# Kernel optimization log

Measured on AMD Instinct MI355X. Metric: run time of the kernel, lower is better.

Reference implementation:

```python
import jax, jax.numpy as jnp
import numpy as np

N_NODES = 8192
N_EDGES = 524288
N_PAIRS = 262144
N_TYPES = 86


def _gcn_conv(x, W, b, src, dst, n):
    # PyG GCNConv: transform, add self-loops, symmetric degree normalization,
    # scatter-add aggregation at destination nodes.
    xw = x @ W  # [N, F_out]
    loop = jnp.arange(n, dtype=src.dtype)
    s = jnp.concatenate([src, loop])
    d = jnp.concatenate([dst, loop])
    deg = jax.ops.segment_sum(jnp.ones(d.shape, xw.dtype), d, num_segments=n)
    dinv = jnp.where(deg > 0, jax.lax.rsqrt(deg), 0.0)  # deg^{-1/2}, 0 for isolated
    coef = dinv[s] * dinv[d]  # [E+N]
    out = jax.ops.segment_sum(xw[s] * coef[:, None], d, num_segments=n)
    return out + b


def setup_inputs() -> dict:
    key = jax.random.key(0)
    ks = jax.random.split(key, 10)
    x = jax.random.normal(ks[0], (N_NODES, N_NODES), dtype=jnp.float32)
    edge_index = jax.random.randint(ks[1], (2, N_EDGES), 0, N_NODES, dtype=jnp.int32)
    drug1_idx = jax.random.randint(ks[2], (N_PAIRS,), 0, N_NODES, dtype=jnp.int32)
    drug2_idx = jax.random.randint(ks[3], (N_PAIRS,), 0, N_NODES, dtype=jnp.int32)
    W1 = jax.random.normal(ks[4], (N_NODES, 128), dtype=jnp.float32) / np.sqrt(N_NODES)
    b1 = jnp.zeros((128,), jnp.float32)
    W2 = jax.random.normal(ks[5], (128, 64), dtype=jnp.float32) / np.sqrt(128.0)
    b2 = jnp.zeros((64,), jnp.float32)
    Wfc = jax.random.normal(ks[6], (128, N_TYPES), dtype=jnp.float32) / np.sqrt(128.0)
    bfc = jnp.zeros((N_TYPES,), jnp.float32)
    return {"x": x, "edge_index": edge_index, "drug1_idx": drug1_idx,
            "drug2_idx": drug2_idx, "W1": W1, "b1": b1, "W2": W2, "b2": b2,
            "Wfc": Wfc, "bfc": bfc}


def reference(x, edge_index, drug1_idx, drug2_idx, W1, b1, W2, b2, Wfc, bfc):
    n = x.shape[0]
    src, dst = edge_index[0], edge_index[1]
    h = jax.nn.relu(_gcn_conv(x, W1, b1, src, dst, n))
    # dropout p=0.3 is identity at inference (training=False)
    h = jax.nn.relu(_gcn_conv(h, W2, b2, src, dst, n))
    combined = jnp.concatenate([h[drug1_idx], h[drug2_idx]], axis=1)  # [P, 128]
    return jax.nn.sigmoid(combined @ Wfc + bfc)
```

## Files before the change

kernel.cpp:

```cpp
#include <hip/hip_runtime.h>
#include <math.h>
#include <stdint.h>
#include <stddef.h>

#define N_NODES 8192
#define N_EDGES 524288
#define N_PAIRS 262144
#define N_TYPES 86
#define F1 128
#define F2 64

typedef unsigned short ushort_t;
typedef unsigned int uint_t;
typedef __attribute__((ext_vector_type(8))) short bfrag;
typedef __attribute__((ext_vector_type(4))) uint_t ufrag;
typedef __attribute__((ext_vector_type(4))) float ffrag;

typedef __attribute__((address_space(3))) char lds_char;
typedef __attribute__((address_space(1))) const char g_char;

__device__ __forceinline__ void gload16(const void* g, void* l) {
  __builtin_amdgcn_global_load_lds((const g_char*)g, (lds_char*)l, 16, 0, 0);
}

__device__ inline ushort_t f2bf(float f) {
  uint_t u = __float_as_uint(f);
  uint_t r = u + 0x7fffu + ((u >> 16) & 1u);
  return (ushort_t)(r >> 16);
}
__device__ inline float bf2f(ushort_t h) {
  return __uint_as_float(((uint_t)h) << 16);
}

__device__ __forceinline__ bfrag cvtfrag(float4 a, float4 b) {
  uint_t h0, h1, h2, h3;
  asm("v_cvt_pk_bf16_f32 %0, %1, %2" : "=v"(h0) : "v"(a.x), "v"(a.y));
  asm("v_cvt_pk_bf16_f32 %0, %1, %2" : "=v"(h1) : "v"(a.z), "v"(a.w));
  asm("v_cvt_pk_bf16_f32 %0, %1, %2" : "=v"(h2) : "v"(b.x), "v"(b.y));
  asm("v_cvt_pk_bf16_f32 %0, %1, %2" : "=v"(h3) : "v"(b.z), "v"(b.w));
  ufrag u;
  u.x = h0; u.y = h1; u.z = h2; u.w = h3;
  return __builtin_bit_cast(bfrag, u);
}


__global__ void zero_k(int* __restrict__ p) {
  p[blockIdx.x * 256 + threadIdx.x] = 0;
}

__global__ void count_deg_k(const int* __restrict__ dst, int* __restrict__ cnt) {
  int e = blockIdx.x * blockDim.x + threadIdx.x;
  if (e < N_EDGES) atomicAdd(&cnt[dst[e]], 1);
}

__global__ void scan_k(const int* __restrict__ cnt, int* __restrict__ rp,
                       int* __restrict__ fill, float* __restrict__ dinv) {
  __shared__ int s[1024];
  int t = threadIdx.x;
  int v[8];
  int sum = 0;
#pragma unroll
  for (int i = 0; i < 8; i++) {
    v[i] = cnt[t * 8 + i];
    dinv[t * 8 + i] = 1.0f / sqrtf((float)(v[i] + 1));
    sum += v[i];
  }
  s[t] = sum;
  __syncthreads();
  for (int off = 1; off < 1024; off <<= 1) {
    int add = (t >= off) ? s[t - off] : 0;
    __syncthreads();
    s[t] += add;
    __syncthreads();
  }
  int excl = s[t] - sum;
#pragma unroll
  for (int i = 0; i < 8; i++) {
    rp[t * 8 + i] = excl;
    fill[t * 8 + i] = excl;
    excl += v[i];
  }
  if (t == 1023) rp[N_NODES] = excl;
}

__global__ void scatter_k(const int* __restrict__ src, const int* __restrict__ dst,
                          int* fill, int* __restrict__ csr) {
  int e = blockIdx.x * blockDim.x + threadIdx.x;
  if (e < N_EDGES) {
    int d = dst[e];
    int pos = atomicAdd(&fill[d], 1);
    csr[pos] = src[e];
  }
}


__global__ __launch_bounds__(256) void w1t_k(const float* __restrict__ W1,
                                             ushort_t* __restrict__ W1t) {
  __shared__ ushort_t lh[32 * 65];
  int tid = threadIdx.x;
  int k0 = blockIdx.x * 64;
  int n0 = blockIdx.y * 32;
#pragma unroll
  for (int i = 0; i < 8; i++) {
    int c = tid + 256 * i;
    int kr = c >> 5, nc = c & 31;
    lh[nc * 65 + kr] = f2bf(W1[(size_t)(k0 + kr) * F1 + n0 + nc]);
  }
  __syncthreads();
  {
    int c = tid;
    int nr = c >> 3, kc = c & 7;
    uint4 u;
    u.x = (uint_t)lh[nr * 65 + kc * 8 + 0] | ((uint_t)lh[nr * 65 + kc * 8 + 1] << 16);
    u.y = (uint_t)lh[nr * 65 + kc * 8 + 2] | ((uint_t)lh[nr * 65 + kc * 8 + 3] << 16);
    u.z = (uint_t)lh[nr * 65 + kc * 8 + 4] | ((uint_t)lh[nr * 65 + kc * 8 + 5] << 16);
    u.w = (uint_t)lh[nr * 65 + kc * 8 + 6] | ((uint_t)lh[nr * 65 + kc * 8 + 7] << 16);
    *(uint4*)(W1t + (size_t)(n0 + nr) * N_NODES + k0 + kc * 8) = u;
  }
}


#define BLDS(b) ((b) * 8192)

#define SCHED0 __builtin_amdgcn_sched_barrier(0)
#define WAITVM(N)  do { asm volatile("s_waitcnt vmcnt(" #N ")" ::: "memory"); SCHED0; } while (0)

__global__ __launch_bounds__(256, 2) void gemm1_mfma_k(const float* __restrict__ x,
                                                       const ushort_t* __restrict__ W1t,
                                                       float* __restrict__ part, int kspan) {
  __shared__ __align__(16) char lds[16384];
  int tid = threadIdx.x;
  int wave = tid >> 6, lane = tid & 63;
  int wr = wave >> 1, wc = wave & 1;
  int lrow = lane & 15, kgrp = lane >> 4;
  int m_blk = blockIdx.y * 128;
  int kbase = blockIdx.x * kspan;
  int ktiles = kspan >> 5;
  int s0 = (5 * blockIdx.y + 3 * blockIdx.x) & (ktiles - 1);

  const float* ap0 = x + (size_t)(m_blk + wr * 64 + 0 * 16 + lrow) * N_NODES + kgrp * 8;
  const float* ap1 = x + (size_t)(m_blk + wr * 64 + 1 * 16 + lrow) * N_NODES + kgrp * 8;
  const float* ap2 = x + (size_t)(m_blk + wr * 64 + 2 * 16 + lrow) * N_NODES + kgrp * 8;
  const float* ap3 = x + (size_t)(m_blk + wr * 64 + 3 * 16 + lrow) * N_NODES + kgrp * 8;

  int bq = wave;
  int b_row = bq * 32 + (lane >> 2);
  int b_kel = ((lane & 3) ^ ((lane >> 2) & 3)) << 3;

  ffrag acc[4][4];
#pragma unroll
  for (int mi = 0; mi < 4; mi++)
#pragma unroll
    for (int ni = 0; ni < 4; ni++) acc[mi][ni] = (ffrag)(0.0f);

  float4 sP[8], sQ[8];
  bfrag afr[4];

#define ISSUE_A(KO, SET)                                                             \
  {                                                                                  \
    SET[0] = *(const float4*)(ap0 + (KO));                                           \
    SET[1] = *(const float4*)(ap0 + (KO) + 4);                                       \
    SET[2] = *(const float4*)(ap1 + (KO));                                           \
    SET[3] = *(const float4*)(ap1 + (KO) + 4);                                       \
    SET[4] = *(const float4*)(ap2 + (KO));                                           \
    SET[5] = *(const float4*)(ap2 + (KO) + 4);                                       \
    SET[6] = *(const float4*)(ap3 + (KO));                                           \
    SET[7] = *(const float4*)(ap3 + (KO) + 4);                                       \
  }

#define CONV(SET)                                                                    \
  {                                                                                  \
    afr[0] = cvtfrag(SET[0], SET[1]);                                                \
    afr[1] = cvtfrag(SET[2], SET[3]);                                                \
    afr[2] = cvtfrag(SET[4], SET[5]);                                                \
    afr[3] = cvtfrag(SET[6], SET[7]);                                                \
  }

#define ISSUE_B(K0, BSEL)                                                            \
  {                                                                                  \
    _Pragma("unroll") for (int i = 0; i < 2; i++) {                                  \
      const ushort_t* gp = W1t + (size_t)(b_row + i * 16) * N_NODES + (K0) + b_kel;  \
      gload16(gp, lds + BLDS(BSEL) + bq * 2048 + i * 1024);                          \
    }                                                                                \
  }

#define COMPUTE(BSEL)                                                                \
  {                                                                                  \
    bfrag bh[4];                                                                     \
    _Pragma("unroll") for (int ni = 0; ni < 4; ni++) {                               \
      int brow = wc * 64 + ni * 16 + lrow;                                           \
      uint_t boff = brow * 64 + ((kgrp ^ (brow & 3)) << 4);                          \
      bh[ni] = *(const bfrag*)(lds + BLDS(BSEL) + boff);                             \
    }                                                                                \
    _Pragma("unroll") for (int mi = 0; mi < 4; mi++) {                               \
      _Pragma("unroll") for (int ni = 0; ni < 4; ni++) {                             \
        acc[mi][ni] = __builtin_amdgcn_mfma_f32_16x16x32_bf16(afr[mi], bh[ni], acc[mi][ni], 0, 0, 0); \
      }                                                                              \
    }                                                                                \
  }

#define NXT(p) ((p) + 1 == ktiles ? 0 : (p) + 1)

  int p1 = s0;
  int p2 = NXT(p1);
  ISSUE_A(kbase + (p1 << 5), sP);
  SCHED0;
  ISSUE_B(kbase + (p1 << 5), 0);
  SCHED0;
  ISSUE_A(kbase + (p2 << 5), sQ);
  WAITVM(10);
  CONV(sP);
  WAITVM(8);
  __builtin_amdgcn_s_barrier();
  SCHED0;

  for (int it = 0; it < ktiles; it += 2) {
    {
      int pB = NXT(p1), pA = NXT(pB);
      ISSUE_B(kbase + (pB << 5), 1);
      SCHED0;
      ISSUE_A(kbase + (pA << 5), sP);
      SCHED0;
      __builtin_amdgcn_s_setprio(1);
      COMPUTE(0);
      __builtin_amdgcn_s_setprio(0);
      WAITVM(10);
      CONV(sQ);
      WAITVM(8);
      __builtin_amdgcn_s_barrier();
      SCHED0;
      p1 = pB;
    }
    {
      int pB = NXT(p1), pA = NXT(pB);
      ISSUE_B(kbase + (pB << 5), 0);
      SCHED0;
      ISSUE_A(kbase + (pA << 5), sQ);
      SCHED0;
      __builtin_amdgcn_s_setprio(1);
      COMPUTE(1);
      __builtin_amdgcn_s_setprio(0);
      WAITVM(10);
      CONV(sP);
      WAITVM(8);
      __builtin_amdgcn_s_barrier();
      SCHED0;
      p1 = pB;
    }
  }

  float* outp = part + (size_t)blockIdx.x * (N_NODES * F1);
#pragma unroll
  for (int mi = 0; mi < 4; mi++) {
#pragma unroll
    for (int ni = 0; ni < 4; ni++) {
      int col = wc * 64 + ni * 16 + lrow;
#pragma unroll
      for (int r = 0; r < 4; r++) {
        int row = m_blk + wr * 64 + mi * 16 + kgrp * 4 + r;
        outp[(size_t)row * F1 + col] = acc[mi][ni][r];
      }
    }
  }
#undef ISSUE_A
#undef CONV
#undef ISSUE_B
#undef COMPUTE
#undef NXT
}

__global__ void reduceS_k(const float* __restrict__ part, float* __restrict__ xw1, int S) {
  int i = blockIdx.x * blockDim.x + threadIdx.x;
  float4 a = ((const float4*)part)[i];
  for (int s = 1; s < S; s++) {
    float4 b = ((const float4*)(part + (size_t)s * N_NODES * F1))[i];
    a.x += b.x; a.y += b.y; a.z += b.z; a.w += b.w;
  }
  ((float4*)xw1)[i] = a;
}


template <int F>
__global__ void agg_k(const float* __restrict__ xw, const int* __restrict__ csr,
                      const int* __restrict__ rp, const float* __restrict__ dinv,
                      const float* __restrict__ bias, float* __restrict__ hout) {
  int node = blockIdx.x;
  int f = threadIdx.x;
  __shared__ int sidx[F];
  __shared__ float sdv[F];
  int beg = rp[node], end = rp[node + 1];
  float acc = 0.f;
  for (int base = beg; base < end; base += F) {
    int n = end - base;
    if (n > F) n = F;
    __syncthreads();
    if (f < n) {
      int s = csr[base + f];
      sidx[f] = s;
      sdv[f] = dinv[s];
    }
    __syncthreads();
    for (int i = 0; i < n; i++) acc += xw[(size_t)sidx[i] * F + f] * sdv[i];
  }
  float dv = dinv[node];
  float v = (acc + xw[(size_t)node * F + f] * dv) * dv + bias[f];
  hout[(size_t)node * F + f] = v > 0.f ? v : 0.f;
}


__global__ __launch_bounds__(256) void gemm2_k(const float* __restrict__ h1,
                                               const float* __restrict__ W2,
                                               float* __restrict__ xw2) {
  __shared__ float W2s[F1 * F2];
  __shared__ float As[16 * F1];
  int tid = threadIdx.x;
  int r0 = blockIdx.x * 16;
#pragma unroll
  for (int j = 0; j < 8; j++)
    ((float4*)W2s)[tid + 256 * j] = ((const float4*)W2)[tid + 256 * j];
#pragma unroll
  for (int j = 0; j < 2; j++)
    ((float4*)As)[tid + 256 * j] = ((const float4*)(h1 + (size_t)r0 * F1))[tid + 256 * j];
  __syncthreads();
  int r = tid >> 4, c4 = tid & 15;
  float4 acc = make_float4(0.f, 0.f, 0.f, 0.f);
#pragma unroll 8
  for (int k = 0; k < F1; k++) {
    float a = As[r * F1 + k];
    float4 bv = *(float4*)&W2s[k * F2 + 4 * c4];
    acc.x += a * bv.x; acc.y += a * bv.y; acc.z += a * bv.z; acc.w += a * bv.w;
  }
  *(float4*)&xw2[(size_t)(r0 + r) * F2 + 4 * c4] = acc;
}


__global__ void pboth_k(const float* __restrict__ h2, const float* __restrict__ Wfc,
                        float* __restrict__ P) {
  __shared__ float hs[64 * 16];
  int tid = threadIdx.x;
  int r0 = blockIdx.x * 16;
  for (int idx = tid; idx < 256; idx += 192) {
    int row = idx >> 4, k4 = idx & 15;
    float4 h = *(const float4*)&h2[(size_t)(r0 + row) * F2 + 4 * k4];
    hs[(4 * k4 + 0) * 16 + row] = h.x;
    hs[(4 * k4 + 1) * 16 + row] = h.y;
    hs[(4 * k4 + 2) * 16 + row] = h.z;
    hs[(4 * k4 + 3) * 16 + row] = h.w;
  }
  __syncthreads();
  if (tid < 172) {
    int half = tid < 86 ? 0 : 1;
    int j = tid - 86 * half;
    const float* wp = Wfc + (size_t)(64 * half) * N_TYPES + j;
    float acc[16];
#pragma unroll
    for (int r = 0; r < 16; r++) acc[r] = 0.f;
    for (int k = 0; k < 64; k++) {
      float w = wp[(size_t)k * N_TYPES];
      const float* hk = &hs[k * 16];
#pragma unroll
      for (int r = 0; r < 16; r++) acc[r] += hk[r] * w;
    }
#pragma unroll
    for (int r = 0; r < 16; r++) P[(size_t)(r0 + r) * 172 + tid] = acc[r];
  }
}


__global__ void final_k(const float* __restrict__ P, const int* __restrict__ d1,
                        const int* __restrict__ d2, const float* __restrict__ bfc,
                        float* __restrict__ out) {
  int gid = blockIdx.x * blockDim.x + threadIdx.x;
  if (gid >= N_PAIRS * 43) return;
  int p = gid / 43;
  int j = gid - p * 43;
  int a = d1[p], b = d2[p];
  float2 v1 = *(const float2*)&P[(size_t)a * 172 + 2 * j];
  float2 v2 = *(const float2*)&P[(size_t)b * 172 + 86 + 2 * j];
  float2 bb = *(const float2*)&bfc[2 * j];
  float z0 = v1.x + v2.x + bb.x;
  float z1 = v1.y + v2.y + bb.y;
  float2 o;
  o.x = 1.0f / (1.0f + expf(-z0));
  o.y = 1.0f / (1.0f + expf(-z1));
  *(float2*)&out[(size_t)p * 86 + 2 * j] = o;
}


extern "C" void kernel_launch(void* const* d_in, const int* in_sizes, int n_in,
                              void* d_out, int out_size, void* d_ws, size_t ws_size,
                              hipStream_t stream) {
  const float* x   = (const float*)d_in[0];
  const int*   ei  = (const int*)d_in[1];
  const int*   d1  = (const int*)d_in[2];
  const int*   d2  = (const int*)d_in[3];
  const float* W1  = (const float*)d_in[4];
  const float* b1  = (const float*)d_in[5];
  const float* W2  = (const float*)d_in[6];
  const float* b2  = (const float*)d_in[7];
  const float* Wfc = (const float*)d_in[8];
  const float* bfc = (const float*)d_in[9];
  float* out = (float*)d_out;

  const int* esrc = ei;
  const int* edst = ei + N_EDGES;

  char* w = (char*)d_ws;
  size_t off = 0;
  auto alloc = [&](size_t bytes) -> char* {
    char* p = w + off;
    off += (bytes + 255) & ~(size_t)255;
    return p;
  };
  int*      cnt  = (int*)alloc((size_t)N_NODES * 4);
  float*    dinv = (float*)alloc((size_t)N_NODES * 4);
  int*      rp   = (int*)alloc((size_t)(N_NODES + 1) * 4);
  int*      fill = (int*)alloc((size_t)N_NODES * 4);
  int*      csr  = (int*)alloc((size_t)N_EDGES * 4);
  ushort_t* W1t  = (ushort_t*)alloc((size_t)N_NODES * F1 * 2);
  float*    h1   = (float*)alloc((size_t)N_NODES * F1 * 4);
  float*    xw2  = (float*)alloc((size_t)N_NODES * F2 * 4);
  float*    h2   = (float*)alloc((size_t)N_NODES * F2 * 4);
  float*    P    = (float*)alloc((size_t)N_NODES * 172 * 4);

  size_t partBytes = (size_t)N_NODES * F1 * 4;
  int S = 8;
  while (S > 1 && off + (size_t)S * partBytes > ws_size) S >>= 1;
  float* part = (float*)alloc((size_t)S * partBytes);
  float* xw1 = part;
  if (off > ws_size) return;

  zero_k<<<N_NODES / 256, 256, 0, stream>>>(cnt);
  count_deg_k<<<N_EDGES / 256, 256, 0, stream>>>(edst, cnt);
  scan_k<<<1, 1024, 0, stream>>>(cnt, rp, fill, dinv);
  scatter_k<<<N_EDGES / 256, 256, 0, stream>>>(esrc, edst, fill, csr);

  w1t_k<<<dim3(N_NODES / 64, F1 / 32), 256, 0, stream>>>(W1, W1t);
  gemm1_mfma_k<<<dim3(S, N_NODES / 128), 256, 0, stream>>>(x, W1t, part, N_NODES / S);
  if (S > 1)
    reduceS_k<<<(N_NODES * F1 / 4) / 256, 256, 0, stream>>>(part, xw1, S);
  agg_k<F1><<<N_NODES, F1, 0, stream>>>(xw1, csr, rp, dinv, b1, h1);

  gemm2_k<<<N_NODES / 16, 256, 0, stream>>>(h1, W2, xw2);
  agg_k<F2><<<N_NODES, F2, 0, stream>>>(xw2, csr, rp, dinv, b2, h2);

  pboth_k<<<N_NODES / 16, 192, 0, stream>>>(h2, Wfc, P);
  final_k<<<(N_PAIRS * 43 + 255) / 256, 256, 0, stream>>>(P, d1, d2, bfc, out);
}
```

Measured before the change: 265.5 us.

## Pre-pack x into bf16 tiles in a separate kernel before GEMM1

Adds a pack kernel that reads the fp32 x matrix once, converts it to bf16 and writes it into a tiled layout matching the MFMA fragment order. The GEMM1 kernel then loads ready-made bf16 fragments instead of converting fp32 in the inner loop, and the pipeline drops to simple single-tile prefetch with full vmcnt(0) waits. This costs an extra 256MB read plus 128MB write and a 128MB workspace, and removes the overlap of the previous deeper prefetch, which is a significant risk for a bandwidth-bound GEMM. The split count S is fixed at 8 and no longer adapts to workspace size.

Result: slower. 322.0 us (+21.3%).

```diff
diff --git a/kernel.cpp b/kernel.cpp
--- a/kernel.cpp
+++ b/kernel.cpp
@@ -28,11 +28,8 @@
   uint_t r = u + 0x7fffu + ((u >> 16) & 1u);
   return (ushort_t)(r >> 16);
 }
-__device__ inline float bf2f(ushort_t h) {
-  return __uint_as_float(((uint_t)h) << 16);
-}
-
-__device__ __forceinline__ bfrag cvtfrag(float4 a, float4 b) {
+
+__device__ __forceinline__ ufrag cvt8(float4 a, float4 b) {
   uint_t h0, h1, h2, h3;
   asm("v_cvt_pk_bf16_f32 %0, %1, %2" : "=v"(h0) : "v"(a.x), "v"(a.y));
   asm("v_cvt_pk_bf16_f32 %0, %1, %2" : "=v"(h1) : "v"(a.z), "v"(a.w));
@@ -40,7 +37,7 @@
   asm("v_cvt_pk_bf16_f32 %0, %1, %2" : "=v"(h3) : "v"(b.z), "v"(b.w));
   ufrag u;
   u.x = h0; u.y = h1; u.z = h2; u.w = h3;
-  return __builtin_bit_cast(bfrag, u);
+  return u;
 }
 
 
@@ -120,28 +117,54 @@
 }
 
 
+__global__ __launch_bounds__(256) void pack_k(const float* __restrict__ x,
+                                              ushort_t* __restrict__ xp) {
+  int tid = threadIdx.x;
+  size_t tile = (size_t)(blockIdx.x * 64 + blockIdx.y) * 131072;
+  const float* xb = x + (size_t)(blockIdx.y * 128) * N_NODES + blockIdx.x * 1024;
+  ushort_t* tp = xp + tile;
+#pragma unroll 4
+  for (int i = 0; i < 32; i++) {
+    int c = tid + 256 * i;
+    int row = c >> 6;
+    int kc = c & 63;
+    const float* p = xb + (size_t)row * N_NODES + kc * 16;
+    float4 v0 = *(const float4*)(p + 0);
+    float4 v1 = *(const float4*)(p + 4);
+    float4 v2 = *(const float4*)(p + 8);
+    float4 v3 = *(const float4*)(p + 12);
+    ufrag u0 = cvt8(v0, v1);
+    ufrag u1 = cvt8(v2, v3);
+    int s = kc >> 1;
+    ushort_t* q = tp + s * 4096 + row * 32 + (kc & 1) * 16;
+    *(ufrag*)q = u0;
+    *(ufrag*)(q + 8) = u1;
+  }
+}
+
+
 #define BLDS(b) ((b) * 8192)
-
 #define SCHED0 __builtin_amdgcn_sched_barrier(0)
 #define WAITVM(N)  do { asm volatile("s_waitcnt vmcnt(" #N ")" ::: "memory"); SCHED0; } while (0)
 
-__global__ __launch_bounds__(256, 2) void gemm1_mfma_k(const float* __restrict__ x,
+__global__ __launch_bounds__(256, 2) void gemm1_mfma_k(const ushort_t* __restrict__ xp,
                                                        const ushort_t* __restrict__ W1t,
-                                                       float* __restrict__ part, int kspan) {
+                                                       float* __restrict__ part) {
   __shared__ __align__(16) char lds[16384];
   int tid = threadIdx.x;
   int wave = tid >> 6, lane = tid & 63;
   int wr = wave >> 1, wc = wave & 1;
   int lrow = lane & 15, kgrp = lane >> 4;
   int m_blk = blockIdx.y * 128;
-  int kbase = blockIdx.x * kspan;
-  int ktiles = kspan >> 5;
+  int kbase = blockIdx.x * 1024;
+  const int ktiles = 32;
   int s0 = (5 * blockIdx.y + 3 * blockIdx.x) & (ktiles - 1);
 
-  const float* ap0 = x + (size_t)(m_blk + wr * 64 + 0 * 16 + lrow) * N_NODES + kgrp * 8;
-  const float* ap1 = x + (size_t)(m_blk + wr * 64 + 1 * 16 + lrow) * N_NODES + kgrp * 8;
-  const float* ap2 = x + (size_t)(m_blk + wr * 64 + 2 * 16 + lrow) * N_NODES + kgrp * 8;
-  const float* ap3 = x + (size_t)(m_blk + wr * 64 + 3 * 16 + lrow) * N_NODES + kgrp * 8;
+  const ushort_t* tp = xp + (size_t)(blockIdx.x * 64 + blockIdx.y) * 131072;
+  int aoff0 = (wr * 64 + 0 * 16 + lrow) * 32 + kgrp * 8;
+  int aoff1 = (wr * 64 + 1 * 16 + lrow) * 32 + kgrp * 8;
+  int aoff2 = (wr * 64 + 2 * 16 + lrow) * 32 + kgrp * 8;
+  int aoff3 = (wr * 64 + 3 * 16 + lrow) * 32 + kgrp * 8;
 
   int bq = wave;
   int b_row = bq * 32 + (lane >> 2);
@@ -153,38 +176,27 @@
 #pragma unroll
     for (int ni = 0; ni < 4; ni++) acc[mi][ni] = (ffrag)(0.0f);
 
-  float4 sP[8], sQ[8];
-  bfrag afr[4];
-
-#define ISSUE_A(KO, SET)                                                             \
+  bfrag aP[4], aQ[4];
+
+#define ISSUE_A(P, SET)                                                              \
   {                                                                                  \
-    SET[0] = *(const float4*)(ap0 + (KO));                                           \
-    SET[1] = *(const float4*)(ap0 + (KO) + 4);                                       \
-    SET[2] = *(const float4*)(ap1 + (KO));                                           \
-    SET[3] = *(const float4*)(ap1 + (KO) + 4);                                       \
-    SET[4] = *(const float4*)(ap2 + (KO));                                           \
-    SET[5] = *(const float4*)(ap2 + (KO) + 4);                                       \
-    SET[6] = *(const float4*)(ap3 + (KO));                                           \
-    SET[7] = *(const float4*)(ap3 + (KO) + 4);                                       \
-  }
-
-#define CONV(SET)                                                                    \
+    const ushort_t* b_ = tp + (P) * 4096;                                            \
+    SET[0] = *(const bfrag*)(b_ + aoff0);                                            \
+    SET[1] = *(const bfrag*)(b_ + aoff1);                                            \
+    SET[2] = *(const bfrag*)(b_ + aoff2);                                            \
+    SET[3] = *(const bfrag*)(b_ + aoff3);                                            \
+  }
+
+#define ISSUE_B(P, BSEL)                                                             \
   {                                                                                  \
-    afr[0] = cvtfrag(SET[0], SET[1]);                                                \
-    afr[1] = cvtfrag(SET[2], SET[3]);                                                \
-    afr[2] = cvtfrag(SET[4], SET[5]);                                                \
-    afr[3] = cvtfrag(SET[6], SET[7]);                                                \
-  }
-
-#define ISSUE_B(K0, BSEL)                                                            \
-  {                                                                                  \
+    int k0_ = kbase + ((P) << 5);                                                    \
     _Pragma("unroll") for (int i = 0; i < 2; i++) {                                  \
-      const ushort_t* gp = W1t + (size_t)(b_row + i * 16) * N_NODES + (K0) + b_kel;  \
+      const ushort_t* gp = W1t + (size_t)(b_row + i * 16) * N_NODES + k0_ + b_kel;   \
       gload16(gp, lds + BLDS(BSEL) + bq * 2048 + i * 1024);                          \
     }                                                                                \
   }
 
-#define COMPUTE(BSEL)                                                                \
+#define COMPUTE(BSEL, SET)                                                           \
   {                                                                                  \
     bfrag bh[4];                                                                     \
     _Pragma("unroll") for (int ni = 0; ni < 4; ni++) {                               \
@@ -194,58 +206,55 @@
     }                                                                                \
     _Pragma("unroll") for (int mi = 0; mi < 4; mi++) {                               \
       _Pragma("unroll") for (int ni = 0; ni < 4; ni++) {                             \
-        acc[mi][ni] = __builtin_amdgcn_mfma_f32_16x16x32_bf16(afr[mi], bh[ni], acc[mi][ni], 0, 0, 0); \
+        acc[mi][ni] = __builtin_amdgcn_mfma_f32_16x16x32_bf16(SET[mi], bh[ni], acc[mi][ni], 0, 0, 0); \
       }                                                                              \
     }                                                                                \
   }
 
 #define NXT(p) ((p) + 1 == ktiles ? 0 : (p) + 1)
 
-  int p1 = s0;
-  int p2 = NXT(p1);
-  ISSUE_A(kbase + (p1 << 5), sP);
+  int p = s0;
+  ISSUE_A(p, aP);
   SCHED0;
-  ISSUE_B(kbase + (p1 << 5), 0);
-  SCHED0;
-  ISSUE_A(kbase + (p2 << 5), sQ);
-  WAITVM(10);
-  CONV(sP);
-  WAITVM(8);
+  ISSUE_B(p, 0);
+  WAITVM(0);
   __builtin_amdgcn_s_barrier();
   SCHED0;
 
   for (int it = 0; it < ktiles; it += 2) {
     {
-      int pB = NXT(p1), pA = NXT(pB);
-      ISSUE_B(kbase + (pB << 5), 1);
-      SCHED0;
-      ISSUE_A(kbase + (pA << 5), sP);
-      SCHED0;
+      int pn = NXT(p);
+      int more = (it + 1 < ktiles);
+      if (more) {
+        ISSUE_A(pn, aQ);
+        SCHED0;
+        ISSUE_B(pn, 1);
+        SCHED0;
+      }
       __builtin_amdgcn_s_setprio(1);
-      COMPUTE(0);
+      COMPUTE(0, aP);
       __builtin_amdgcn_s_setprio(0);
-      WAITVM(10);
-      CONV(sQ);
-      WAITVM(8);
+      WAITVM(0);
       __builtin_amdgcn_s_barrier();
       SCHED0;
-      p1 = pB;
+      p = pn;
     }
     {
-      int pB = NXT(p1), pA = NXT(pB);
-      ISSUE_B(kbase + (pB << 5), 0);
-      SCHED0;
-      ISSUE_A(kbase + (pA << 5), sQ);
-      SCHED0;
+      int pn = NXT(p);
+      int more = (it + 2 < ktiles);
+      if (more) {
+        ISSUE_A(pn, aP);
+        SCHED0;
+        ISSUE_B(pn, 0);
+        SCHED0;
+      }
       __builtin_amdgcn_s_setprio(1);
-      COMPUTE(1);
+      COMPUTE(1, aQ);
       __builtin_amdgcn_s_setprio(0);
-      WAITVM(10);
-      CONV(sP);
-      WAITVM(8);
+      WAITVM(0);
       __builtin_amdgcn_s_barrier();
       SCHED0;
-      p1 = pB;
+      p = pn;
     }
   }
 
@@ -263,7 +272,6 @@
     }
   }
 #undef ISSUE_A
-#undef CONV
 #undef ISSUE_B
 #undef COMPUTE
 #undef NXT
@@ -422,10 +430,10 @@
   float*    xw2  = (float*)alloc((size_t)N_NODES * F2 * 4);
   float*    h2   = (float*)alloc((size_t)N_NODES * F2 * 4);
   float*    P    = (float*)alloc((size_t)N_NODES * 172 * 4);
-
+  ushort_t* xp   = (ushort_t*)alloc((size_t)N_NODES * N_NODES * 2);
+
+  const int S = 8;
   size_t partBytes = (size_t)N_NODES * F1 * 4;
-  int S = 8;
-  while (S > 1 && off + (size_t)S * partBytes > ws_size) S >>= 1;
   float* part = (float*)alloc((size_t)S * partBytes);
   float* xw1 = part;
   if (off > ws_size) return;
@@ -436,9 +444,9 @@
   scatter_k<<<N_EDGES / 256, 256, 0, stream>>>(esrc, edst, fill, csr);
 
   w1t_k<<<dim3(N_NODES / 64, F1 / 32), 256, 0, stream>>>(W1, W1t);
-  gemm1_mfma_k<<<dim3(S, N_NODES / 128), 256, 0, stream>>>(x, W1t, part, N_NODES / S);
-  if (S > 1)
-    reduceS_k<<<(N_NODES * F1 / 4) / 256, 256, 0, stream>>>(part, xw1, S);
+  pack_k<<<dim3(S, N_NODES / 128), 256, 0, stream>>>(x, xp);
+  gemm1_mfma_k<<<dim3(S, N_NODES / 128), 256, 0, stream>>>(xp, W1t, part);
+  reduceS_k<<<(N_NODES * F1 / 4) / 256, 256, 0, stream>>>(part, xw1, S);
   agg_k<F1><<<N_NODES, F1, 0, stream>>>(xw1, csr, rp, dinv, b1, h1);
 
   gemm2_k<<<N_NODES / 16, 256, 0, stream>>>(h1, W2, xw2);
```
